# Kernel optimization log

Hardware: AMD Instinct MI355X
Metric: run time of the kernel (lower is better)

Reference implementation:

```python
import jax, jax.numpy as jnp
import numpy as np

# ---- static config (matches module defaults / init_kwargs) ----
SX = 256; SY = 256; C = 3; NK = 12; B = 4
R = 10; DT = 0.2; DD = 5; SIGMA = 0.65; THETA_A = 1.0; N_EXP = 2


def _build_kernels():
    """Replicates compute_kernel(): multi-ring Lenia kernels, normalized in real space."""
    rng = np.random.default_rng(42)
    mid = SX // 2
    g = np.mgrid[-mid:mid, -mid:mid]
    dist = np.linalg.norm(g, axis=0)  # [SX, SY]
    Ks = []
    for _ in range(NK):
        r = rng.uniform(0.3, 1.0)
        a = rng.uniform(0.0, 1.0, 3)
        w = rng.uniform(0.05, 0.2, 3)
        b = rng.uniform(0.0, 1.0, 3)
        D = dist / ((R + 15) * r)
        sig = 1.0 / (1.0 + np.exp((D - 1.0) * 10.0))  # sigmoid(-(D-1)*10)
        kerf = (b[None, None, :] * np.exp(-(((D[..., None] - a[None, None, :]) / w[None, None, :]) ** 2) / 2.0)).sum(-1)
        Ks.append(sig * kerf)
    K = np.stack(Ks, axis=-1)  # [SX, SY, NK]
    Kn = K / K.sum(axis=(0, 1), keepdims=True)
    m = rng.uniform(0.05, 0.5, NK)
    s = rng.uniform(0.01, 0.18, NK)
    h = rng.uniform(0.2, 1.0, NK)
    return (Kn.astype(np.float32), m.astype(np.float32), s.astype(np.float32), h.astype(np.float32))


def setup_inputs() -> dict:
    key = jax.random.key(0)
    Kn, m, s, h = _build_kernels()
    A = jax.random.uniform(key, (B, 1, SX, SY, C), dtype=jnp.float32)
    c0 = jnp.asarray(np.arange(NK) % C, dtype=jnp.int32)      # source channel of each kernel
    c1_map = jnp.asarray(np.arange(NK) % C, dtype=jnp.int32)  # target channel of each kernel
    return {"A": A, "Kn": jnp.asarray(Kn), "m": jnp.asarray(m), "s": jnp.asarray(s),
            "h": jnp.asarray(h), "c0": c0, "c1_map": c1_map}


def _sobel(A):
    """Circular (torus) Sobel, separable [1,2,1]x[-1,0,1]/8, on spatial axes (2,3).
    A: [B,1,SX,SY,C] -> [B,1,SX,SY,2,C] (d/dx, d/dy)."""
    sy = jnp.roll(A, -1, 3) + 2.0 * A + jnp.roll(A, 1, 3)
    gx = (jnp.roll(sy, -1, 2) - jnp.roll(sy, 1, 2)) / 8.0
    sx = jnp.roll(A, -1, 2) + 2.0 * A + jnp.roll(A, 1, 2)
    gy = (jnp.roll(sx, -1, 3) - jnp.roll(sx, 1, 3)) / 8.0
    return jnp.stack([gx, gy], axis=4)


def _forward(A, Kn, m, s, h, c0, c1_map):
    # FFT-domain convolution per kernel
    fK = jnp.fft.fft2(jnp.fft.fftshift(Kn, axes=(0, 1)), axes=(0, 1))  # [SX,SY,NK] complex
    fA = jnp.fft.fft2(A, axes=(2, 3))                                   # [B,1,SX,SY,C]
    fAk = fA[..., c0]                                                    # [B,1,SX,SY,NK]
    U = jnp.fft.ifft2(fK[None, None] * fAk, axes=(2, 3)).real           # [B,1,SX,SY,NK]
    # growth(U,m,s) = 2*bell(U,m,s)-1, scaled by h
    G = (2.0 * jnp.exp(-((U - m) ** 2) / (2.0 * s ** 2)) - 1.0) * h
    # sum kernel contributions into their target channel (c1)
    M = jax.nn.one_hot(c1_map, C, dtype=G.dtype)                         # [NK,C]
    Uc = jnp.einsum('bzxyk,kc->bzxyc', G, M)                             # [B,1,SX,SY,C]
    nabla_U = _sobel(Uc)                                                 # [B,1,SX,SY,2,C]
    nabla_A = _sobel(A.sum(-1, keepdims=True))                           # [B,1,SX,SY,2,1]
    alpha = jnp.clip((A[:, :, :, :, None, :] / THETA_A) ** N_EXP, 0.0, 1.0)
    F = nabla_U * (1.0 - alpha) - nabla_A * alpha                        # flow field
    # ---- reintegration tracking (RT) over a (2*DD+1)^2 neighborhood ----
    x = jnp.arange(SX, dtype=F.dtype); y = jnp.arange(SY, dtype=F.dtype)
    pos = jnp.stack(jnp.meshgrid(x, y, indexing='ij'), axis=-1) + 0.5    # [SX,SY,2]
    ma = DD - SIGMA
    mus = pos[None, None, :, :, :, None] + jnp.clip(DT * F, -ma, ma)     # target centers [B,1,SX,SY,2,C]
    offsets = jnp.asarray([(dx, dy) for dx in range(-DD, DD + 1) for dy in range(-DD, DD + 1)], dtype=jnp.int32)
    amax = min(1.0, 2.0 * SIGMA)

    def body(acc, off):
        dx, dy = off[0], off[1]
        rollA = jnp.roll(A, (dx, dy), axis=(2, 3))
        rollmu = jnp.roll(mus, (dx, dy), axis=(2, 3))
        dpmu = jnp.abs(pos[None, None, :, :, :, None] - rollmu)
        sz = 0.5 - dpmu + SIGMA
        area = jnp.prod(jnp.clip(sz, 0.0, amax), axis=4) / (4.0 * SIGMA ** 2)  # [B,1,SX,SY,C]
        return acc + rollA * area, None

    nA, _ = jax.lax.scan(jax.checkpoint(body), jnp.zeros_like(A), offsets)
    return nA


def reference(A, Kn, m, s, h, c0, c1_map):
    return _forward(A, Kn, m, s, h, c0, c1_map)
```

## Files before the change

### kernel.cpp

```cpp
#include <hip/hip_runtime.h>


typedef _Float16 f16;
typedef __attribute__((ext_vector_type(8))) _Float16 half8;
typedef __attribute__((ext_vector_type(16))) float f32x16;

#define RMAX 44
#define NROWS 89
#define NDMAX 8
#define NFRAG (3*NROWS*NDMAX)
#define ST 168
#define TROWS 120
#define SCHED_STRIDE 1024

__global__ __launch_bounds__(128) void lenia_meta(const float* __restrict__ Kn,
                                                  int2* __restrict__ meta,
                                                  int* __restrict__ rowr) {
    int blk = blockIdx.x;
    int c = blk / NROWS, ri = blk - c * NROWS;
    int di = ri - RMAX;
    int t = threadIdx.x;
    int dj = t - RMAX;
    int act = 0;
    if (t < NROWS) {
        size_t base = (size_t)(((di + 128) << 8) | (dj + 128)) * 12 + c;
        float k0 = Kn[base], k1 = Kn[base + 3], k2 = Kn[base + 6], k3 = Kn[base + 9];
        act = (fmaxf(fmaxf(k0, k1), fmaxf(k2, k3)) > 1e-9f) ? 1 : 0;
    }
    __shared__ int smn[128], smx[128];
    smn[t] = act ? dj : 1000;
    smx[t] = act ? dj : -1000;
    __syncthreads();
    for (int s = 64; s > 0; s >>= 1) {
        if (t < s) { smn[t] = min(smn[t], smn[t + s]); smx[t] = max(smx[t], smx[t + s]); }
        __syncthreads();
    }
    if (t == 0) {
        int jmn = smn[0], jmx = smx[0];
        if (jmx < jmn) { meta[blk] = make_int2(1, 0); rowr[blk] = 0; }
        else {
            meta[blk] = make_int2(jmn, jmx);
            rowr[blk] = max(abs(di), max(abs(jmn), abs(jmx)));
        }
    }
}

__global__ __launch_bounds__(128) void lenia_sched(const int2* __restrict__ meta,
                                                   const int* __restrict__ rowr,
                                                   int2* __restrict__ meta2,
                                                   unsigned int* __restrict__ sched,
                                                   int* __restrict__ nsched,
                                                   int* __restrict__ radii) {
    int c = blockIdx.x;
    int t = threadIdx.x;
    __shared__ int pre[NROWS], nds[NROWS], rmx[128];
    int nd = 0, d0 = 0;
    if (t < NROWS) {
        int2 bm = meta[c * NROWS + t];
        if (bm.y >= bm.x) {
            d0 = ((bm.x - 7) >> 3) << 3;
            nd = ((bm.y + 7 - d0) >> 4) + 1;
        }
        meta2[c * NROWS + t] = make_int2(d0, nd);
        nds[t] = nd;
    }
    rmx[t] = (t < NROWS) ? rowr[c * NROWS + t] : 0;
    __syncthreads();
    for (int s = 64; s > 0; s >>= 1) {
        if (t < s) rmx[t] = max(rmx[t], rmx[t + s]);
        __syncthreads();
    }
    __shared__ int tot;
    if (t == 0) {
        radii[c] = rmx[0];
        int acc = 0;
        for (int i = 0; i < NROWS; ++i) { pre[i] = acc; acc += nds[i]; }
        tot = acc;
    }
    __syncthreads();
    if (t < NROWS && nd > 0) {
        int base = pre[t];
        for (int i = 0; i < nd; ++i) {
            int delta = d0 + 16 * i;
            unsigned int off = (unsigned int)(t * ST + delta + 128);
            sched[c * SCHED_STRIDE + base + i] =
                (unsigned int)((c * NROWS + t) * NDMAX + i) | (off << 12);
        }
    }
    if (t == 0) {
        int ns = (tot + 7) & ~7;
        unsigned int padoff = (unsigned int)(RMAX * ST + 128);
        for (int i = tot; i < ns + 24; ++i)
            sched[c * SCHED_STRIDE + i] = (unsigned int)NFRAG | (padoff << 12);
        nsched[c] = ns;
    }
}

__global__ __launch_bounds__(256) void lenia_trans(const float* __restrict__ Kn,
                                                   const float* __restrict__ A,
                                                   f16* __restrict__ Ktr,
                                                   f16* __restrict__ Atr) {
    int blk = blockIdx.x, tid = threadIdx.x;
    if (blk < 256) {
        int gid = blk * 256 + tid;
        const float4* kp = (const float4*)(Kn + (size_t)gid * 12);
        float4 v0 = kp[0], v1 = kp[1], v2 = kp[2];
        Ktr[0 * 65536 + gid]  = (f16)v0.x;  Ktr[1 * 65536 + gid]  = (f16)v0.y;
        Ktr[2 * 65536 + gid]  = (f16)v0.z;  Ktr[3 * 65536 + gid]  = (f16)v0.w;
        Ktr[4 * 65536 + gid]  = (f16)v1.x;  Ktr[5 * 65536 + gid]  = (f16)v1.y;
        Ktr[6 * 65536 + gid]  = (f16)v1.z;  Ktr[7 * 65536 + gid]  = (f16)v1.w;
        Ktr[8 * 65536 + gid]  = (f16)v2.x;  Ktr[9 * 65536 + gid]  = (f16)v2.y;
        Ktr[10 * 65536 + gid] = (f16)v2.z;  Ktr[11 * 65536 + gid] = (f16)v2.w;
    } else {
        int px = (blk - 256) * 256 + tid;
        int b = px >> 16, rem = px & 65535;
        const float* ap = A + (size_t)px * 3;
        Atr[(size_t)(b * 3 + 0) * 65536 + rem] = (f16)ap[0];
        Atr[(size_t)(b * 3 + 1) * 65536 + rem] = (f16)ap[1];
        Atr[(size_t)(b * 3 + 2) * 65536 + rem] = (f16)ap[2];
    }
}

__global__ __launch_bounds__(256) void lenia_bpack(const f16* __restrict__ Ktr,
                                                   const int2* __restrict__ meta2,
                                                   uint4* __restrict__ bpack) {
    int fi = blockIdx.x * 4 + (threadIdx.x >> 6);
    int l = threadIdx.x & 63;
    if (fi > NFRAG) return;
    union { f16 h[8]; uint4 u; } pk;
    if (fi == NFRAG) {
        pk.u = make_uint4(0, 0, 0, 0);
        bpack[(size_t)fi * 64 + l] = pk.u;
        return;
    }
    int c = fi / (NROWS * NDMAX);
    int rem = fi - c * (NROWS * NDMAX);
    int ri = rem >> 3, didx = rem & 7;
    int di = ri - RMAX;
    int delta = meta2[c * NROWS + ri].x + 16 * didx;
    int q = (l & 31) >> 3, sy = l & 7, g = l >> 5;
    int dj0 = delta + 8 * g - sy;
    const f16* src = Ktr + (size_t)(c + 3 * q) * 65536 + ((di + 128) << 8) + (dj0 + 128);
    #pragma unroll
    for (int j = 0; j < 8; ++j) pk.h[j] = src[j];
    bpack[(size_t)fi * 64 + l] = pk.u;
}

__global__ __launch_bounds__(256) void lenia_conv(
        const f16* __restrict__ Atr, const uint4* __restrict__ bpack,
        const unsigned int* __restrict__ sched, const int* __restrict__ nsched,
        const int* __restrict__ radii,
        const float* __restrict__ mp, const float* __restrict__ sp,
        const float* __restrict__ hp, f16* __restrict__ Uc) {
    extern __shared__ f16 smh[];

    const int tid = threadIdx.x;
    const int bc = blockIdx.y;
    const int b = bc / 3, c = bc - b * 3;
    const int x0 = (blockIdx.x >> 3) << 5;
    const int y0 = (blockIdx.x & 7) << 5;

    const int R = __builtin_amdgcn_readfirstlane(min(max(radii[c], 1), RMAX));
    const int R8 = (R + 7) & ~7;
    const int colbase = y0 - R8 - 16;
    const int rows = 32 + 2 * R;
    const f16* Ap = Atr + (size_t)(b * 3 + c) * 65536;

    {
        int nchunk = rows * 21;
        int tr = tid / 21, rem = tid - tr * 21;
        for (int ci = tid; ci < nchunk; ci += 256) {
            int gi = (x0 - R + tr) & 255;
            int gj = (colbase + rem * 8) & 255;
            *(half8*)(smh + tr * ST + rem * 8) = *(const half8*)(Ap + (gi << 8) + gj);
            tr += 12; rem += 4;
            if (rem >= 21) { rem -= 21; ++tr; }
        }
    }
    __syncthreads();

    const int lane = tid & 63, wid = tid >> 6;
    const int m = lane & 31, g = lane >> 5;
    const int abase = (m + R - RMAX) * ST + 8 * wid + R8 + 16 + 8 * g;

    const unsigned int* schedC = sched + c * SCHED_STRIDE;
    const int ns = __builtin_amdgcn_readfirstlane(nsched[c]);

    f32x16 accE, accO;
    #pragma unroll
    for (int r = 0; r < 16; ++r) { accE[r] = 0.f; accO[r] = 0.f; }

    unsigned int eq[8];
    uint4 bq[8];
    #pragma unroll
    for (int j = 0; j < 8; ++j) {
        eq[j] = schedC[j];
        bq[j] = bpack[(size_t)(eq[j] & 4095u) * 64 + lane];
    }

    for (int it = 0; it < ns; it += 8) {
        #pragma unroll
        for (int j = 0; j < 8; j += 2) {
            {
                half8 av = *(const half8*)(smh + abase + ((int)(eq[j] >> 12) - 128));
                union { uint4 u; half8 h; } bb; bb.u = bq[j];
                accE = __builtin_amdgcn_mfma_f32_32x32x16_f16(av, bb.h, accE, 0, 0, 0);
                unsigned int ne = schedC[it + 8 + j];
                eq[j] = ne;
                bq[j] = bpack[(size_t)(ne & 4095u) * 64 + lane];
            }
            {
                half8 av = *(const half8*)(smh + abase + ((int)(eq[j + 1] >> 12) - 128));
                union { uint4 u; half8 h; } bb; bb.u = bq[j + 1];
                accO = __builtin_amdgcn_mfma_f32_32x32x16_f16(av, bb.h, accO, 0, 0, 0);
                unsigned int ne = schedC[it + 8 + j + 1];
                eq[j + 1] = ne;
                bq[j + 1] = bpack[(size_t)(ne & 4095u) * 64 + lane];
            }
        }
    }

    const int q = (lane & 31) >> 3, sy = lane & 7;
    const float mq = mp[c + 3 * q];
    const float sq = sp[c + 3 * q];
    const float hq = hp[c + 3 * q];
    const float i2s = 1.f / (2.f * sq * sq);
    #pragma unroll
    for (int r = 0; r < 16; ++r) {
        float d = (accE[r] + accO[r]) - mq;
        float gg = (2.f * expf(-d * d * i2s) - 1.f) * hq;
        gg += __shfl_xor(gg, 8);
        gg += __shfl_xor(gg, 16);
        if ((lane & 24) == 0) {
            int row = (r & 3) + ((r >> 2) << 3) + (g << 2);
            Uc[((size_t)(b << 16) + ((x0 + row) << 8) + (y0 + 8 * wid + sy)) * 3 + c] = (f16)gg;
        }
    }
}

#define FTW 44
#define FSW 45
#define PLH (FSW * FTW)
__global__ __launch_bounds__(256) void lenia_flowrt(
        const float* __restrict__ A, const f16* __restrict__ Uc,
        float* __restrict__ out) {
    extern __shared__ char fraw[];
    f16*    ucp = (f16*)fraw;
    f16*    atp = (f16*)(fraw + 3 * PLH * 2);
    float4* mqp = (float4*)(fraw + 6 * PLH * 2);

    int b = blockIdx.y, t = blockIdx.x;
    int x0 = (t >> 3) << 5, y0 = (t & 7) << 5;
    const float* Ab = A  + ((size_t)b << 16) * 3;
    const f16*   Ub = Uc + ((size_t)b << 16) * 3;

    for (int idx = threadIdx.x; idx < FTW * FTW; idx += 256) {
        int si = idx / FTW, sj = idx - si * FTW;
        int gi = (x0 - 6 + si) & 255, gj = (y0 - 6 + sj) & 255;
        size_t p = (size_t)((gi << 8) + gj) * 3;
        int o = si * FSW + sj;
        ucp[o] = Ub[p]; ucp[PLH + o] = Ub[p + 1]; ucp[2 * PLH + o] = Ub[p + 2];
        atp[o] = (f16)Ab[p]; atp[PLH + o] = (f16)Ab[p + 1]; atp[2 * PLH + o] = (f16)Ab[p + 2];
    }
    __syncthreads();

    for (int idx = threadIdx.x; idx < 42 * 42; idx += 256) {
        int ci = idx / 42, cj = idx - ci * 42;
        int si = ci + 1, sj = cj + 1;
        int o = si * FSW + sj;
        int vx = x0 - 6 + si, vy = y0 - 6 + sj;
        float sx = (vx < 0 || vx > 255) ? 1e7f : 0.f;
        float syv = (vy < 0 || vy > 255) ? 1e7f : 0.f;

        float as[3][3];
        #pragma unroll
        for (int i = 0; i < 3; ++i)
            #pragma unroll
            for (int j = 0; j < 3; ++j) {
                int oo = o + (i - 1) * FSW + (j - 1);
                as[i][j] = (float)atp[oo] + (float)atp[PLH + oo] + (float)atp[2 * PLH + oo];
            }
        float gxA = ((as[2][0] + 2.f * as[2][1] + as[2][2])
                   - (as[0][0] + 2.f * as[0][1] + as[0][2])) * 0.125f;
        float gyA = ((as[0][2] + 2.f * as[1][2] + as[2][2])
                   - (as[0][0] + 2.f * as[1][0] + as[2][0])) * 0.125f;

        #pragma unroll
        for (int c = 0; c < 3; ++c) {
            const f16* up = ucp + c * PLH;
            float u00 = up[o - FSW - 1], u01 = up[o - FSW], u02 = up[o - FSW + 1];
            float u10 = up[o - 1],                        u12 = up[o + 1];
            float u20 = up[o + FSW - 1], u21 = up[o + FSW], u22 = up[o + FSW + 1];
            float gx = ((u20 + 2.f * u21 + u22) - (u00 + 2.f * u01 + u02)) * 0.125f;
            float gy = ((u02 + 2.f * u12 + u22) - (u00 + 2.f * u10 + u20)) * 0.125f;
            float a = (float)atp[c * PLH + o];
            float alpha = fminf(a * a, 1.f);
            float Fx = gx * (1.f - alpha) - gxA * alpha;
            float Fy = gy * (1.f - alpha) - gyA * alpha;
            float dx = fminf(fmaxf(0.2f * Fx, -4.35f), 4.35f) + sx;
            float dy = fminf(fmaxf(0.2f * Fy, -4.35f), 4.35f) + syv;
            mqp[c * PLH + o] = make_float4(dx, dy, a, 0.f);
        }
    }
    __syncthreads();

    int tx = threadIdx.x & 31, tyg = threadIdx.x >> 5;
    int ty0 = tyg << 2;
    float acc[3][4] = {};

    for (int dxs = 0; dxs < 11; ++dxs) {
        float fdx = (float)(5 - dxs);
        int rowb = (tx + 1 + dxs) * FSW + (ty0 + 1);
        #pragma unroll
        for (int sjj = 0; sjj < 14; ++sjj) {
            float fdy = (float)(5 - sjj);
            #pragma unroll
            for (int c = 0; c < 3; ++c) {
                float4 qv = mqp[c * PLH + rowb + sjj];
                float wx = fminf(fmaxf(1.15f - fabsf(fdx - qv.x), 0.f), 1.f);
                float awx = qv.z * wx;
                float e0 = fdy - qv.y;
                acc[c][0] = fmaf(awx, fminf(fmaxf(1.15f - fabsf(e0), 0.f), 1.f), acc[c][0]);
                acc[c][1] = fmaf(awx, fminf(fmaxf(1.15f - fabsf(e0 + 1.f), 0.f), 1.f), acc[c][1]);
                acc[c][2] = fmaf(awx, fminf(fmaxf(1.15f - fabsf(e0 + 2.f), 0.f), 1.f), acc[c][2]);
                acc[c][3] = fmaf(awx, fminf(fmaxf(1.15f - fabsf(e0 + 3.f), 0.f), 1.f), acc[c][3]);
            }
        }
    }
    const float inv = 1.0f / 1.69f;
    #pragma unroll
    for (int tt = 0; tt < 4; ++tt) {
        size_t o = ((size_t)(b << 16) + ((x0 + tx) << 8) + (y0 + ty0 + tt)) * 3;
        out[o]     = acc[0][tt] * inv;
        out[o + 1] = acc[1][tt] * inv;
        out[o + 2] = acc[2][tt] * inv;
    }
}

extern "C" void kernel_launch(void* const* d_in, const int* in_sizes, int n_in,
                              void* d_out, int out_size, void* d_ws, size_t ws_size,
                              hipStream_t stream) {
    const float* A  = (const float*)d_in[0];
    const float* Kn = (const float*)d_in[1];
    const float* m  = (const float*)d_in[2];
    const float* s  = (const float*)d_in[3];
    const float* h  = (const float*)d_in[4];

    char* ws = (char*)d_ws;
    int*          radii = (int*)ws;
    int*          nschd = (int*)(ws + 16);
    int*          rowr  = (int*)(ws + 64);
    int2*         meta  = (int2*)(ws + 2048);
    int2*         meta2 = (int2*)(ws + 8192);
    unsigned int* sched = (unsigned int*)(ws + 16384);
    f16*          Ktr   = (f16*)(ws + 32768);
    f16*          Atr   = (f16*)(ws + 1605632);
    uint4*        bpack = (uint4*)(ws + 3178496);
    f16*          Uc    = (f16*)(ws + 32768);

    lenia_meta<<<3 * NROWS, 128, 0, stream>>>(Kn, meta, rowr);
    lenia_sched<<<3, 128, 0, stream>>>(meta, rowr, meta2, sched, nschd, radii);
    lenia_trans<<<1280, 256, 0, stream>>>(Kn, A, Ktr, Atr);
    lenia_bpack<<<(NFRAG + 4) / 4, 256, 0, stream>>>(Ktr, meta2, bpack);
    lenia_conv<<<dim3(64, 12), 256, TROWS * ST * sizeof(f16), stream>>>(
        Atr, bpack, sched, nschd, radii, m, s, h, Uc);
    lenia_flowrt<<<dim3(64, 4), 256, (6 * PLH * 2) + (3 * PLH * 16), stream>>>(
        A, Uc, (float*)d_out);
}
```

Baseline: 82.29 us.

## Split kernel schedule across waves with 4-column B-fragment reuse and LDS reduction

The conv kernel now has each wave process a quarter of the fragment schedule across all four 8-column octets. Each loaded B fragment feeds four MFMAs instead of one, which cuts global bpack loads per MFMA. Partial accumulators are combined through a two-step shared-memory tree reduction before the Gaussian growth epilogue. The kernel-activity threshold is also raised from 1e-9 to 1e-7 to trim kernel support, and the schedule is padded to a multiple of 32; the higher threshold drops small kernel taps, which changes results slightly.

Measured after the change: 86.14 us. +4.7%, slower.

```diff
diff --git a/kernel.cpp b/kernel.cpp
--- a/kernel.cpp
+++ b/kernel.cpp
@@ -12,6 +12,7 @@
 #define ST 168
 #define TROWS 120
 #define SCHED_STRIDE 1024
+#define KTHR 1e-7f
 
 __global__ __launch_bounds__(128) void lenia_meta(const float* __restrict__ Kn,
                                                   int2* __restrict__ meta,
@@ -25,7 +26,7 @@
     if (t < NROWS) {
         size_t base = (size_t)(((di + 128) << 8) | (dj + 128)) * 12 + c;
         float k0 = Kn[base], k1 = Kn[base + 3], k2 = Kn[base + 6], k3 = Kn[base + 9];
-        act = (fmaxf(fmaxf(k0, k1), fmaxf(k2, k3)) > 1e-9f) ? 1 : 0;
+        act = (fmaxf(fmaxf(k0, k1), fmaxf(k2, k3)) > KTHR) ? 1 : 0;
     }
     __shared__ int smn[128], smx[128];
     smn[t] = act ? dj : 1000;
@@ -88,9 +89,9 @@
         }
     }
     if (t == 0) {
-        int ns = (tot + 7) & ~7;
+        int ns = (tot + 31) & ~31;
         unsigned int padoff = (unsigned int)(RMAX * ST + 128);
-        for (int i = tot; i < ns + 24; ++i)
+        for (int i = tot; i < ns + 32; ++i)
             sched[c * SCHED_STRIDE + i] = (unsigned int)NFRAG | (padoff << 12);
         nsched[c] = ns;
     }
@@ -181,59 +182,99 @@
 
     const int lane = tid & 63, wid = tid >> 6;
     const int m = lane & 31, g = lane >> 5;
-    const int abase = (m + R - RMAX) * ST + 8 * wid + R8 + 16 + 8 * g;
-
-    const unsigned int* schedC = sched + c * SCHED_STRIDE;
+    const int abase = (m + R - RMAX) * ST + R8 + 16 + 8 * g - 128;
+
     const int ns = __builtin_amdgcn_readfirstlane(nsched[c]);
-
-    f32x16 accE, accO;
+    const int q4 = ns >> 2;
+    const unsigned int* sW = sched + c * SCHED_STRIDE + wid * q4;
+
+    f32x16 acc0, acc1, acc2, acc3;
     #pragma unroll
-    for (int r = 0; r < 16; ++r) { accE[r] = 0.f; accO[r] = 0.f; }
+    for (int r = 0; r < 16; ++r) { acc0[r] = 0.f; acc1[r] = 0.f; acc2[r] = 0.f; acc3[r] = 0.f; }
 
     unsigned int eq[8];
     uint4 bq[8];
     #pragma unroll
     for (int j = 0; j < 8; ++j) {
-        eq[j] = schedC[j];
+        eq[j] = sW[j];
         bq[j] = bpack[(size_t)(eq[j] & 4095u) * 64 + lane];
     }
 
-    for (int it = 0; it < ns; it += 8) {
-        #pragma unroll
-        for (int j = 0; j < 8; j += 2) {
-            {
-                half8 av = *(const half8*)(smh + abase + ((int)(eq[j] >> 12) - 128));
-                union { uint4 u; half8 h; } bb; bb.u = bq[j];
-                accE = __builtin_amdgcn_mfma_f32_32x32x16_f16(av, bb.h, accE, 0, 0, 0);
-                unsigned int ne = schedC[it + 8 + j];
-                eq[j] = ne;
-                bq[j] = bpack[(size_t)(ne & 4095u) * 64 + lane];
+    for (int it = 0; it < q4; it += 8) {
+        #pragma unroll
+        for (int j = 0; j < 8; ++j) {
+            const int off = abase + (int)(eq[j] >> 12);
+            half8 a0 = *(const half8*)(smh + off);
+            half8 a1 = *(const half8*)(smh + off + 8);
+            half8 a2 = *(const half8*)(smh + off + 16);
+            half8 a3 = *(const half8*)(smh + off + 24);
+            union { uint4 u; half8 h; } bb; bb.u = bq[j];
+            acc0 = __builtin_amdgcn_mfma_f32_32x32x16_f16(a0, bb.h, acc0, 0, 0, 0);
+            acc1 = __builtin_amdgcn_mfma_f32_32x32x16_f16(a1, bb.h, acc1, 0, 0, 0);
+            acc2 = __builtin_amdgcn_mfma_f32_32x32x16_f16(a2, bb.h, acc2, 0, 0, 0);
+            acc3 = __builtin_amdgcn_mfma_f32_32x32x16_f16(a3, bb.h, acc3, 0, 0, 0);
+            unsigned int ne = sW[it + 8 + j];
+            eq[j] = ne;
+            bq[j] = bpack[(size_t)(ne & 4095u) * 64 + lane];
+        }
+    }
+
+    __syncthreads();
+    float* red = (float*)smh;
+    if (wid & 1) {
+        float* dst = red + (wid >> 1) * (64 * 65) + lane * 65;
+        #pragma unroll
+        for (int r = 0; r < 16; ++r) {
+            dst[r] = acc0[r]; dst[16 + r] = acc1[r];
+            dst[32 + r] = acc2[r]; dst[48 + r] = acc3[r];
+        }
+    }
+    __syncthreads();
+    if (!(wid & 1)) {
+        const float* src = red + (wid >> 1) * (64 * 65) + lane * 65;
+        #pragma unroll
+        for (int r = 0; r < 16; ++r) {
+            acc0[r] += src[r]; acc1[r] += src[16 + r];
+            acc2[r] += src[32 + r]; acc3[r] += src[48 + r];
+        }
+    }
+    __syncthreads();
+    if (wid == 2) {
+        float* dst = red + lane * 65;
+        #pragma unroll
+        for (int r = 0; r < 16; ++r) {
+            dst[r] = acc0[r]; dst[16 + r] = acc1[r];
+            dst[32 + r] = acc2[r]; dst[48 + r] = acc3[r];
+        }
+    }
+    __syncthreads();
+    if (wid == 0) {
+        const float* src = red + lane * 65;
+        #pragma unroll
+        for (int r = 0; r < 16; ++r) {
+            acc0[r] += src[r]; acc1[r] += src[16 + r];
+            acc2[r] += src[32 + r]; acc3[r] += src[48 + r];
+        }
+        const int q = (lane & 31) >> 3, sy = lane & 7;
+        const float mq = mp[c + 3 * q];
+        const float sq = sp[c + 3 * q];
+        const float hq = hp[c + 3 * q];
+        const float i2s = 1.f / (2.f * sq * sq);
+        #pragma unroll
+        for (int oct = 0; oct < 4; ++oct) {
+            const f32x16& acc = (oct == 0) ? acc0 : (oct == 1) ? acc1 : (oct == 2) ? acc2 : acc3;
+            const int col = y0 + 8 * oct + sy;
+            #pragma unroll
+            for (int r = 0; r < 16; ++r) {
+                float d = acc[r] - mq;
+                float gg = (2.f * expf(-d * d * i2s) - 1.f) * hq;
+                gg += __shfl_xor(gg, 8);
+                gg += __shfl_xor(gg, 16);
+                if ((lane & 24) == 0) {
+                    int row = (r & 3) + ((r >> 2) << 3) + (g << 2);
+                    Uc[((size_t)(b << 16) + ((x0 + row) << 8) + col) * 3 + c] = (f16)gg;
+                }
             }
-            {
-                half8 av = *(const half8*)(smh + abase + ((int)(eq[j + 1] >> 12) - 128));
-                union { uint4 u; half8 h; } bb; bb.u = bq[j + 1];
-                accO = __builtin_amdgcn_mfma_f32_32x32x16_f16(av, bb.h, accO, 0, 0, 0);
-                unsigned int ne = schedC[it + 8 + j + 1];
-                eq[j + 1] = ne;
-                bq[j + 1] = bpack[(size_t)(ne & 4095u) * 64 + lane];
-            }
-        }
-    }
-
-    const int q = (lane & 31) >> 3, sy = lane & 7;
-    const float mq = mp[c + 3 * q];
-    const float sq = sp[c + 3 * q];
-    const float hq = hp[c + 3 * q];
-    const float i2s = 1.f / (2.f * sq * sq);
-    #pragma unroll
-    for (int r = 0; r < 16; ++r) {
-        float d = (accE[r] + accO[r]) - mq;
-        float gg = (2.f * expf(-d * d * i2s) - 1.f) * hq;
-        gg += __shfl_xor(gg, 8);
-        gg += __shfl_xor(gg, 16);
-        if ((lane & 24) == 0) {
-            int row = (r & 3) + ((r >> 2) << 3) + (g << 2);
-            Uc[((size_t)(b << 16) + ((x0 + row) << 8) + (y0 + 8 * wid + sy)) * 3 + c] = (f16)gg;
         }
     }
 }
```

## Split conv halo staging into two phases to shrink LDS footprint

Applied to the files above, without the earlier changes.

The convolution kernel now stages the input tile in two passes: rows for kernel offsets up to zero, then the remaining rows. The schedule is split accordingly, so LDS per block drops from 120 to 76 rows, which should let more blocks co-reside per CU. In exchange there is an extra barrier and a second global-to-LDS load phase. The kernel-support threshold is also raised from 1e-9 to 1e-7, trimming more near-zero kernel taps at a small accuracy cost.

New measurement: 89.98 us. +9.4%, slower.

```diff
diff --git a/kernel.cpp b/kernel.cpp
--- a/kernel.cpp
+++ b/kernel.cpp
@@ -10,8 +10,9 @@
 #define NDMAX 8
 #define NFRAG (3*NROWS*NDMAX)
 #define ST 168
-#define TROWS 120
+#define PROWS 76
 #define SCHED_STRIDE 1024
+#define KTHR 1e-7f
 
 __global__ __launch_bounds__(128) void lenia_meta(const float* __restrict__ Kn,
                                                   int2* __restrict__ meta,
@@ -25,7 +26,7 @@
     if (t < NROWS) {
         size_t base = (size_t)(((di + 128) << 8) | (dj + 128)) * 12 + c;
         float k0 = Kn[base], k1 = Kn[base + 3], k2 = Kn[base + 6], k3 = Kn[base + 9];
-        act = (fmaxf(fmaxf(k0, k1), fmaxf(k2, k3)) > 1e-9f) ? 1 : 0;
+        act = (fmaxf(fmaxf(k0, k1), fmaxf(k2, k3)) > KTHR) ? 1 : 0;
     }
     __shared__ int smn[128], smx[128];
     smn[t] = act ? dj : 1000;
@@ -49,11 +50,12 @@
                                                    const int* __restrict__ rowr,
                                                    int2* __restrict__ meta2,
                                                    unsigned int* __restrict__ sched,
-                                                   int* __restrict__ nsched,
+                                                   int2* __restrict__ nsched,
                                                    int* __restrict__ radii) {
     int c = blockIdx.x;
     int t = threadIdx.x;
     __shared__ int pre[NROWS], nds[NROWS], rmx[128];
+    __shared__ int s_R, s_ns0, s_tot0;
     int nd = 0, d0 = 0;
     if (t < NROWS) {
         int2 bm = meta[c * NROWS + t];
@@ -70,29 +72,36 @@
         if (t < s) rmx[t] = max(rmx[t], rmx[t + s]);
         __syncthreads();
     }
-    __shared__ int tot;
     if (t == 0) {
+        int R = max(1, min(rmx[0], RMAX));
         radii[c] = rmx[0];
+        s_R = R;
         int acc = 0;
         for (int i = 0; i < NROWS; ++i) { pre[i] = acc; acc += nds[i]; }
-        tot = acc;
+        int tot0 = pre[RMAX] + nds[RMAX];
+        int tot1 = acc - tot0;
+        int ns0 = (tot0 + 7) & ~7;
+        int ns1 = (tot1 + 7) & ~7;
+        s_ns0 = ns0; s_tot0 = tot0;
+        nsched[c] = make_int2(ns0, ns1);
+        unsigned int* sc = sched + c * SCHED_STRIDE;
+        unsigned int pad0 = (unsigned int)NFRAG | ((unsigned int)(R * ST + 128) << 12);
+        unsigned int pad1 = (unsigned int)NFRAG | (128u << 12);
+        for (int i = tot0; i < ns0; ++i) sc[i] = pad0;
+        for (int i = ns0 + tot1; i < ns0 + ns1 + 16; ++i) sc[i] = pad1;
     }
     __syncthreads();
     if (t < NROWS && nd > 0) {
-        int base = pre[t];
+        int R = s_R, ns0 = s_ns0, tot0 = s_tot0;
+        int di = t - RMAX;
+        int base   = (t <= RMAX) ? pre[t] : ns0 + (pre[t] - tot0);
+        int rowoff = (t <= RMAX) ? (di + R) * ST : (di - 1) * ST;
         for (int i = 0; i < nd; ++i) {
             int delta = d0 + 16 * i;
-            unsigned int off = (unsigned int)(t * ST + delta + 128);
+            unsigned int off = (unsigned int)(rowoff + delta + 128);
             sched[c * SCHED_STRIDE + base + i] =
                 (unsigned int)((c * NROWS + t) * NDMAX + i) | (off << 12);
         }
-    }
-    if (t == 0) {
-        int ns = (tot + 7) & ~7;
-        unsigned int padoff = (unsigned int)(RMAX * ST + 128);
-        for (int i = tot; i < ns + 24; ++i)
-            sched[c * SCHED_STRIDE + i] = (unsigned int)NFRAG | (padoff << 12);
-        nsched[c] = ns;
     }
 }
 
@@ -148,7 +157,7 @@
 
 __global__ __launch_bounds__(256) void lenia_conv(
         const f16* __restrict__ Atr, const uint4* __restrict__ bpack,
-        const unsigned int* __restrict__ sched, const int* __restrict__ nsched,
+        const unsigned int* __restrict__ sched, const int2* __restrict__ nsched,
         const int* __restrict__ radii,
         const float* __restrict__ mp, const float* __restrict__ sp,
         const float* __restrict__ hp, f16* __restrict__ Uc) {
@@ -163,59 +172,68 @@
     const int R = __builtin_amdgcn_readfirstlane(min(max(radii[c], 1), RMAX));
     const int R8 = (R + 7) & ~7;
     const int colbase = y0 - R8 - 16;
-    const int rows = 32 + 2 * R;
     const f16* Ap = Atr + (size_t)(b * 3 + c) * 65536;
-
-    {
-        int nchunk = rows * 21;
-        int tr = tid / 21, rem = tid - tr * 21;
-        for (int ci = tid; ci < nchunk; ci += 256) {
-            int gi = (x0 - R + tr) & 255;
-            int gj = (colbase + rem * 8) & 255;
-            *(half8*)(smh + tr * ST + rem * 8) = *(const half8*)(Ap + (gi << 8) + gj);
-            tr += 12; rem += 4;
-            if (rem >= 21) { rem -= 21; ++tr; }
-        }
-    }
-    __syncthreads();
 
     const int lane = tid & 63, wid = tid >> 6;
     const int m = lane & 31, g = lane >> 5;
-    const int abase = (m + R - RMAX) * ST + 8 * wid + R8 + 16 + 8 * g;
-
+    const int abase = m * ST + 8 * wid + R8 + 16 + 8 * g - 128;
+
+    const int2 nsv = nsched[c];
+    const int ns0 = __builtin_amdgcn_readfirstlane(nsv.x);
+    const int ns1 = __builtin_amdgcn_readfirstlane(nsv.y);
     const unsigned int* schedC = sched + c * SCHED_STRIDE;
-    const int ns = __builtin_amdgcn_readfirstlane(nsched[c]);
 
     f32x16 accE, accO;
     #pragma unroll
     for (int r = 0; r < 16; ++r) { accE[r] = 0.f; accO[r] = 0.f; }
 
-    unsigned int eq[8];
-    uint4 bq[8];
-    #pragma unroll
-    for (int j = 0; j < 8; ++j) {
-        eq[j] = schedC[j];
-        bq[j] = bpack[(size_t)(eq[j] & 4095u) * 64 + lane];
-    }
-
-    for (int it = 0; it < ns; it += 8) {
+    for (int phase = 0; phase < 2; ++phase) {
+        const int rowBase = phase ? (x0 + 1) : (x0 - R);
+        const int nrows   = phase ? (R + 31) : (R + 32);
+        const int nsP     = phase ? ns1 : ns0;
+        const unsigned int* sW = phase ? (schedC + ns0) : schedC;
+
+        if (phase) __syncthreads();
+        {
+            int nchunk = nrows * 21;
+            int tr = tid / 21, rem = tid - tr * 21;
+            for (int ci = tid; ci < nchunk; ci += 256) {
+                int gi = (rowBase + tr) & 255;
+                int gj = (colbase + rem * 8) & 255;
+                *(half8*)(smh + tr * ST + rem * 8) = *(const half8*)(Ap + (gi << 8) + gj);
+                tr += 12; rem += 4;
+                if (rem >= 21) { rem -= 21; ++tr; }
+            }
+        }
+        __syncthreads();
+
+        unsigned int eq[8];
+        uint4 bq[8];
         #pragma unroll
-        for (int j = 0; j < 8; j += 2) {
-            {
-                half8 av = *(const half8*)(smh + abase + ((int)(eq[j] >> 12) - 128));
-                union { uint4 u; half8 h; } bb; bb.u = bq[j];
-                accE = __builtin_amdgcn_mfma_f32_32x32x16_f16(av, bb.h, accE, 0, 0, 0);
-                unsigned int ne = schedC[it + 8 + j];
-                eq[j] = ne;
-                bq[j] = bpack[(size_t)(ne & 4095u) * 64 + lane];
-            }
-            {
-                half8 av = *(const half8*)(smh + abase + ((int)(eq[j + 1] >> 12) - 128));
-                union { uint4 u; half8 h; } bb; bb.u = bq[j + 1];
-                accO = __builtin_amdgcn_mfma_f32_32x32x16_f16(av, bb.h, accO, 0, 0, 0);
-                unsigned int ne = schedC[it + 8 + j + 1];
-                eq[j + 1] = ne;
-                bq[j + 1] = bpack[(size_t)(ne & 4095u) * 64 + lane];
+        for (int j = 0; j < 8; ++j) {
+            eq[j] = sW[j];
+            bq[j] = bpack[(size_t)(eq[j] & 4095u) * 64 + lane];
+        }
+
+        for (int it = 0; it < nsP; it += 8) {
+            #pragma unroll
+            for (int j = 0; j < 8; j += 2) {
+                {
+                    half8 av = *(const half8*)(smh + abase + (int)(eq[j] >> 12));
+                    union { uint4 u; half8 h; } bb; bb.u = bq[j];
+                    accE = __builtin_amdgcn_mfma_f32_32x32x16_f16(av, bb.h, accE, 0, 0, 0);
+                    unsigned int ne = sW[it + 8 + j];
+                    eq[j] = ne;
+                    bq[j] = bpack[(size_t)(ne & 4095u) * 64 + lane];
+                }
+                {
+                    half8 av = *(const half8*)(smh + abase + (int)(eq[j + 1] >> 12));
+                    union { uint4 u; half8 h; } bb; bb.u = bq[j + 1];
+                    accO = __builtin_amdgcn_mfma_f32_32x32x16_f16(av, bb.h, accO, 0, 0, 0);
+                    unsigned int ne = sW[it + 9 + j];
+                    eq[j + 1] = ne;
+                    bq[j + 1] = bpack[(size_t)(ne & 4095u) * 64 + lane];
+                }
             }
         }
     }
@@ -348,7 +366,7 @@
 
     char* ws = (char*)d_ws;
     int*          radii = (int*)ws;
-    int*          nschd = (int*)(ws + 16);
+    int2*         nschd = (int2*)(ws + 16);
     int*          rowr  = (int*)(ws + 64);
     int2*         meta  = (int2*)(ws + 2048);
     int2*         meta2 = (int2*)(ws + 8192);
@@ -362,7 +380,7 @@
     lenia_sched<<<3, 128, 0, stream>>>(meta, rowr, meta2, sched, nschd, radii);
     lenia_trans<<<1280, 256, 0, stream>>>(Kn, A, Ktr, Atr);
     lenia_bpack<<<(NFRAG + 4) / 4, 256, 0, stream>>>(Ktr, meta2, bpack);
-    lenia_conv<<<dim3(64, 12), 256, TROWS * ST * sizeof(f16), stream>>>(
+    lenia_conv<<<dim3(64, 12), 256, PROWS * ST * sizeof(f16), stream>>>(
         Atr, bpack, sched, nschd, radii, m, s, h, Uc);
     lenia_flowrt<<<dim3(64, 4), 256, (6 * PLH * 2) + (3 * PLH * 16), stream>>>(
         A, Uc, (float*)d_out);
```

## Split flow/RT kernel per channel, deepen conv prefetch, raise kernel sparsity threshold

Applied to the files above, without the earlier changes.

The flow/reintegration kernel now launches one block per (batch, channel, tile), giving three times as many blocks with smaller shared memory. Each block stores only a float2 mu per pixel and reads A from the fp16 transposed buffer instead of the fp32 input. The conv MFMA loop prefetches 16 schedule entries instead of 8, with padding extended to match. The kernel-activity threshold rises from 1e-9 to 1e-7, which prunes more near-zero kernel taps at some accuracy risk. The per-channel split also recomputes the A gradient three times.

Measured after the change: 74.95 us. 8.9% less time.

```diff
diff --git a/kernel.cpp b/kernel.cpp
--- a/kernel.cpp
+++ b/kernel.cpp
@@ -12,6 +12,7 @@
 #define ST 168
 #define TROWS 120
 #define SCHED_STRIDE 1024
+#define KTHR 1e-7f
 
 __global__ __launch_bounds__(128) void lenia_meta(const float* __restrict__ Kn,
                                                   int2* __restrict__ meta,
@@ -25,7 +26,7 @@
     if (t < NROWS) {
         size_t base = (size_t)(((di + 128) << 8) | (dj + 128)) * 12 + c;
         float k0 = Kn[base], k1 = Kn[base + 3], k2 = Kn[base + 6], k3 = Kn[base + 9];
-        act = (fmaxf(fmaxf(k0, k1), fmaxf(k2, k3)) > 1e-9f) ? 1 : 0;
+        act = (fmaxf(fmaxf(k0, k1), fmaxf(k2, k3)) > KTHR) ? 1 : 0;
     }
     __shared__ int smn[128], smx[128];
     smn[t] = act ? dj : 1000;
@@ -90,7 +91,7 @@
     if (t == 0) {
         int ns = (tot + 7) & ~7;
         unsigned int padoff = (unsigned int)(RMAX * ST + 128);
-        for (int i = tot; i < ns + 24; ++i)
+        for (int i = tot; i < ns + 48; ++i)
             sched[c * SCHED_STRIDE + i] = (unsigned int)NFRAG | (padoff << 12);
         nsched[c] = ns;
     }
@@ -181,39 +182,39 @@
 
     const int lane = tid & 63, wid = tid >> 6;
     const int m = lane & 31, g = lane >> 5;
-    const int abase = (m + R - RMAX) * ST + 8 * wid + R8 + 16 + 8 * g;
-
-    const unsigned int* schedC = sched + c * SCHED_STRIDE;
+    const int abase = (m + R - RMAX) * ST + 8 * wid + R8 + 16 + 8 * g - 128;
+
+    const unsigned int* sW = sched + c * SCHED_STRIDE;
     const int ns = __builtin_amdgcn_readfirstlane(nsched[c]);
 
     f32x16 accE, accO;
     #pragma unroll
     for (int r = 0; r < 16; ++r) { accE[r] = 0.f; accO[r] = 0.f; }
 
-    unsigned int eq[8];
-    uint4 bq[8];
+    unsigned int eq[16];
+    uint4 bq[16];
     #pragma unroll
-    for (int j = 0; j < 8; ++j) {
-        eq[j] = schedC[j];
+    for (int j = 0; j < 16; ++j) {
+        eq[j] = sW[j];
         bq[j] = bpack[(size_t)(eq[j] & 4095u) * 64 + lane];
     }
 
-    for (int it = 0; it < ns; it += 8) {
+    for (int it = 0; it < ns; it += 16) {
         #pragma unroll
-        for (int j = 0; j < 8; j += 2) {
+        for (int j = 0; j < 16; j += 2) {
             {
-                half8 av = *(const half8*)(smh + abase + ((int)(eq[j] >> 12) - 128));
+                half8 av = *(const half8*)(smh + abase + (int)(eq[j] >> 12));
                 union { uint4 u; half8 h; } bb; bb.u = bq[j];
                 accE = __builtin_amdgcn_mfma_f32_32x32x16_f16(av, bb.h, accE, 0, 0, 0);
-                unsigned int ne = schedC[it + 8 + j];
+                unsigned int ne = sW[it + 16 + j];
                 eq[j] = ne;
                 bq[j] = bpack[(size_t)(ne & 4095u) * 64 + lane];
             }
             {
-                half8 av = *(const half8*)(smh + abase + ((int)(eq[j + 1] >> 12) - 128));
+                half8 av = *(const half8*)(smh + abase + (int)(eq[j + 1] >> 12));
                 union { uint4 u; half8 h; } bb; bb.u = bq[j + 1];
                 accO = __builtin_amdgcn_mfma_f32_32x32x16_f16(av, bb.h, accO, 0, 0, 0);
-                unsigned int ne = schedC[it + 8 + j + 1];
+                unsigned int ne = sW[it + 17 + j];
                 eq[j + 1] = ne;
                 bq[j + 1] = bpack[(size_t)(ne & 4095u) * 64 + lane];
             }
@@ -242,25 +243,29 @@
 #define FSW 45
 #define PLH (FSW * FTW)
 __global__ __launch_bounds__(256) void lenia_flowrt(
-        const float* __restrict__ A, const f16* __restrict__ Uc,
+        const f16* __restrict__ Atr, const f16* __restrict__ Uc,
         float* __restrict__ out) {
     extern __shared__ char fraw[];
     f16*    ucp = (f16*)fraw;
-    f16*    atp = (f16*)(fraw + 3 * PLH * 2);
-    float4* mqp = (float4*)(fraw + 6 * PLH * 2);
-
-    int b = blockIdx.y, t = blockIdx.x;
+    f16*    atp = (f16*)(fraw + PLH * 2);
+    float2* muq = (float2*)(fraw + 8 * PLH);
+
+    int bc = blockIdx.y;
+    int b = bc / 3, c = bc - b * 3;
+    int t = blockIdx.x;
     int x0 = (t >> 3) << 5, y0 = (t & 7) << 5;
-    const float* Ab = A  + ((size_t)b << 16) * 3;
-    const f16*   Ub = Uc + ((size_t)b << 16) * 3;
+    const f16* A0 = Atr + (size_t)(b * 3) * 65536;
+    const f16* Ub = Uc + ((size_t)b << 16) * 3;
 
     for (int idx = threadIdx.x; idx < FTW * FTW; idx += 256) {
         int si = idx / FTW, sj = idx - si * FTW;
         int gi = (x0 - 6 + si) & 255, gj = (y0 - 6 + sj) & 255;
-        size_t p = (size_t)((gi << 8) + gj) * 3;
+        int pix = (gi << 8) + gj;
         int o = si * FSW + sj;
-        ucp[o] = Ub[p]; ucp[PLH + o] = Ub[p + 1]; ucp[2 * PLH + o] = Ub[p + 2];
-        atp[o] = (f16)Ab[p]; atp[PLH + o] = (f16)Ab[p + 1]; atp[2 * PLH + o] = (f16)Ab[p + 2];
+        ucp[o] = Ub[(size_t)pix * 3 + c];
+        atp[o] = A0[pix];
+        atp[PLH + o] = A0[65536 + pix];
+        atp[2 * PLH + o] = A0[131072 + pix];
     }
     __syncthreads();
 
@@ -285,28 +290,25 @@
         float gyA = ((as[0][2] + 2.f * as[1][2] + as[2][2])
                    - (as[0][0] + 2.f * as[1][0] + as[2][0])) * 0.125f;
 
-        #pragma unroll
-        for (int c = 0; c < 3; ++c) {
-            const f16* up = ucp + c * PLH;
-            float u00 = up[o - FSW - 1], u01 = up[o - FSW], u02 = up[o - FSW + 1];
-            float u10 = up[o - 1],                        u12 = up[o + 1];
-            float u20 = up[o + FSW - 1], u21 = up[o + FSW], u22 = up[o + FSW + 1];
-            float gx = ((u20 + 2.f * u21 + u22) - (u00 + 2.f * u01 + u02)) * 0.125f;
-            float gy = ((u02 + 2.f * u12 + u22) - (u00 + 2.f * u10 + u20)) * 0.125f;
-            float a = (float)atp[c * PLH + o];
-            float alpha = fminf(a * a, 1.f);
-            float Fx = gx * (1.f - alpha) - gxA * alpha;
-            float Fy = gy * (1.f - alpha) - gyA * alpha;
-            float dx = fminf(fmaxf(0.2f * Fx, -4.35f), 4.35f) + sx;
-            float dy = fminf(fmaxf(0.2f * Fy, -4.35f), 4.35f) + syv;
-            mqp[c * PLH + o] = make_float4(dx, dy, a, 0.f);
-        }
+        float u00 = ucp[o - FSW - 1], u01 = ucp[o - FSW], u02 = ucp[o - FSW + 1];
+        float u10 = ucp[o - 1],                          u12 = ucp[o + 1];
+        float u20 = ucp[o + FSW - 1], u21 = ucp[o + FSW], u22 = ucp[o + FSW + 1];
+        float gx = ((u20 + 2.f * u21 + u22) - (u00 + 2.f * u01 + u02)) * 0.125f;
+        float gy = ((u02 + 2.f * u12 + u22) - (u00 + 2.f * u10 + u20)) * 0.125f;
+        float a = (float)atp[c * PLH + o];
+        float alpha = fminf(a * a, 1.f);
+        float Fx = gx * (1.f - alpha) - gxA * alpha;
+        float Fy = gy * (1.f - alpha) - gyA * alpha;
+        float dx = fminf(fmaxf(0.2f * Fx, -4.35f), 4.35f) + sx;
+        float dy = fminf(fmaxf(0.2f * Fy, -4.35f), 4.35f) + syv;
+        muq[o] = make_float2(dx, dy);
     }
     __syncthreads();
 
     int tx = threadIdx.x & 31, tyg = threadIdx.x >> 5;
     int ty0 = tyg << 2;
-    float acc[3][4] = {};
+    float a0 = 0.f, a1 = 0.f, a2 = 0.f, a3 = 0.f;
+    const f16* ac = atp + c * PLH;
 
     for (int dxs = 0; dxs < 11; ++dxs) {
         float fdx = (float)(5 - dxs);
@@ -314,27 +316,23 @@
         #pragma unroll
         for (int sjj = 0; sjj < 14; ++sjj) {
             float fdy = (float)(5 - sjj);
-            #pragma unroll
-            for (int c = 0; c < 3; ++c) {
-                float4 qv = mqp[c * PLH + rowb + sjj];
-                float wx = fminf(fmaxf(1.15f - fabsf(fdx - qv.x), 0.f), 1.f);
-                float awx = qv.z * wx;
-                float e0 = fdy - qv.y;
-                acc[c][0] = fmaf(awx, fminf(fmaxf(1.15f - fabsf(e0), 0.f), 1.f), acc[c][0]);
-                acc[c][1] = fmaf(awx, fminf(fmaxf(1.15f - fabsf(e0 + 1.f), 0.f), 1.f), acc[c][1]);
-                acc[c][2] = fmaf(awx, fminf(fmaxf(1.15f - fabsf(e0 + 2.f), 0.f), 1.f), acc[c][2]);
-                acc[c][3] = fmaf(awx, fminf(fmaxf(1.15f - fabsf(e0 + 3.f), 0.f), 1.f), acc[c][3]);
-            }
+            float2 mu = muq[rowb + sjj];
+            float av = (float)ac[rowb + sjj];
+            float wx = fminf(fmaxf(1.15f - fabsf(fdx - mu.x), 0.f), 1.f);
+            float awx = av * wx;
+            float e0 = fdy - mu.y;
+            a0 = fmaf(awx, fminf(fmaxf(1.15f - fabsf(e0), 0.f), 1.f), a0);
+            a1 = fmaf(awx, fminf(fmaxf(1.15f - fabsf(e0 + 1.f), 0.f), 1.f), a1);
+            a2 = fmaf(awx, fminf(fmaxf(1.15f - fabsf(e0 + 2.f), 0.f), 1.f), a2);
+            a3 = fmaf(awx, fminf(fmaxf(1.15f - fabsf(e0 + 3.f), 0.f), 1.f), a3);
         }
     }
     const float inv = 1.0f / 1.69f;
-    #pragma unroll
-    for (int tt = 0; tt < 4; ++tt) {
-        size_t o = ((size_t)(b << 16) + ((x0 + tx) << 8) + (y0 + ty0 + tt)) * 3;
-        out[o]     = acc[0][tt] * inv;
-        out[o + 1] = acc[1][tt] * inv;
-        out[o + 2] = acc[2][tt] * inv;
-    }
+    size_t ob = ((size_t)(b << 16) + ((x0 + tx) << 8) + (y0 + ty0)) * 3 + c;
+    out[ob]     = a0 * inv;
+    out[ob + 3] = a1 * inv;
+    out[ob + 6] = a2 * inv;
+    out[ob + 9] = a3 * inv;
 }
 
 extern "C" void kernel_launch(void* const* d_in, const int* in_sizes, int n_in,
@@ -364,6 +362,6 @@
     lenia_bpack<<<(NFRAG + 4) / 4, 256, 0, stream>>>(Ktr, meta2, bpack);
     lenia_conv<<<dim3(64, 12), 256, TROWS * ST * sizeof(f16), stream>>>(
         Atr, bpack, sched, nschd, radii, m, s, h, Uc);
-    lenia_flowrt<<<dim3(64, 4), 256, (6 * PLH * 2) + (3 * PLH * 16), stream>>>(
-        A, Uc, (float*)d_out);
-}
+    lenia_flowrt<<<dim3(64, 12), 256, 8 * PLH + PLH * 8, stream>>>(
+        Atr, Uc, (float*)d_out);
+}
```
